# Performance work log

Measured on AMD Instinct MI355X. Metric: run time of the kernel, lower is better.

The kernel has to match this reference:

```python
import jax, jax.numpy as jnp
import numpy as np

B, T, D, H, L, FF, SPLIT = 2, 4096, 256, 4 * 0 + 8, 4, 1024, 2048
HD = D // H
EPS = 1e-5


def _layernorm(x, s, b):
    mu = jnp.mean(x, axis=-1, keepdims=True)
    var = jnp.mean(jnp.square(x - mu), axis=-1, keepdims=True)
    return (x - mu) * jax.lax.rsqrt(var + EPS) * s + b


def setup_inputs() -> dict:
    key = jax.random.key(0)
    ks = jax.random.split(key, 10)
    sc = 0.02
    inp = {
        "rows": jax.random.normal(ks[0], (B, T, D), jnp.float32),
        "train_target_embeddings": jax.random.normal(ks[1], (B, SPLIT, D), jnp.float32),
        "Wq": sc * jax.random.normal(ks[2], (L, D, D), jnp.float32),
        "bq": jnp.zeros((L, D), jnp.float32),
        "Wk": sc * jax.random.normal(ks[3], (L, D, D), jnp.float32),
        "bk": jnp.zeros((L, D), jnp.float32),
        "Wv": sc * jax.random.normal(ks[4], (L, D, D), jnp.float32),
        "bv": jnp.zeros((L, D), jnp.float32),
        "Wo": sc * jax.random.normal(ks[5], (L, D, D), jnp.float32),
        "bo": jnp.zeros((L, D), jnp.float32),
        "W1": sc * jax.random.normal(ks[6], (L, D, FF), jnp.float32),
        "b1": jnp.zeros((L, FF), jnp.float32),
        "W2": sc * jax.random.normal(ks[7], (L, FF, D), jnp.float32),
        "b2": jnp.zeros((L, D), jnp.float32),
        "ln1_s": jnp.ones((L, D), jnp.float32),
        "ln1_b": jnp.zeros((L, D), jnp.float32),
        "ln2_s": jnp.ones((L, D), jnp.float32),
        "ln2_b": jnp.zeros((L, D), jnp.float32),
        "split": SPLIT,
    }
    return inp


def reference(rows, train_target_embeddings, Wq, bq, Wk, bk, Wv, bv, Wo, bo,
              W1, b1, W2, b2, ln1_s, ln1_b, ln2_s, ln2_b, split):
    # residual add of train target embeddings onto the train rows
    x = rows.at[:, :split, :].add(train_target_embeddings)
    t = x.shape[1]
    # allowed mask: every query can see all train columns; test queries also see themselves
    key_is_train = jnp.arange(t) < split                      # [T]
    allowed = key_is_train[None, :] | jnp.eye(t, dtype=bool)  # [T,T]
    neg = jnp.asarray(-1e9, x.dtype)
    scale = 1.0 / np.sqrt(HD)
    n_layers = Wq.shape[0]
    for l in range(n_layers):
        # multi-head attention with structured mask
        q = (x @ Wq[l] + bq[l]).reshape(x.shape[0], t, H, HD)
        k = (x @ Wk[l] + bk[l]).reshape(x.shape[0], t, H, HD)
        v = (x @ Wv[l] + bv[l]).reshape(x.shape[0], t, H, HD)
        logits = jnp.einsum('bqhd,bkhd->bhqk', q, k) * scale
        logits = jnp.where(allowed[None, None], logits, neg)
        attn = jax.nn.softmax(logits, axis=-1)
        o = jnp.einsum('bhqk,bkhd->bqhd', attn, v).reshape(x.shape[0], t, D)
        x = _layernorm(x + (o @ Wo[l] + bo[l]), ln1_s[l], ln1_b[l])
        # feed-forward
        h = jax.nn.gelu(x @ W1[l] + b1[l])
        x = _layernorm(x + (h @ W2[l] + b2[l]), ln2_s[l], ln2_b[l])
    return x
```

## Files before the change

### kernel.cpp

```cpp
#include <hip/hip_runtime.h>
#include <cstdint>
#include <cstddef>

#define TSEQ 4096
#define BATCH 2
#define DIM 256
#define NHEAD 8
#define HDIM 32
#define NLAYER 4
#define FFDIM 1024
#define SPLITN 2048
#define MROWS (BATCH * TSEQ)

#define QSCALE 0.2550784545f

typedef __attribute__((ext_vector_type(4))) float f32x4;
typedef __attribute__((ext_vector_type(8))) short bf16x8;

__device__ __forceinline__ short f2bf(float f) {
  union { float f; uint32_t u; } v; v.f = f;
  uint32_t r = v.u + 0x7fffu + ((v.u >> 16) & 1u);
  return (short)(r >> 16);
}

__device__ __forceinline__ float fast_exp2(float x) {
#if __has_builtin(__builtin_amdgcn_exp2f)
  return __builtin_amdgcn_exp2f(x);
#else
  float r;
  asm volatile("v_exp_f32 %0, %1\n\ts_nop 1" : "=v"(r) : "v"(x));
  return r;
#endif
}

__device__ __forceinline__ uint32_t pack2bf(float a, float b) {
  union { float f; uint32_t u; } ua, ub; ua.f = a; ub.f = b;
  return ((ua.u + 0x8000u) >> 16) | ((ub.u + 0x8000u) & 0xffff0000u);
}

__device__ __forceinline__ float gelu_f(float x) {
  float u = 0.7978845608f * x * (1.0f + 0.044715f * x * x);
  u = fminf(fmaxf(u, -20.f), 20.f);
  float e = fast_exp2(2.885390082f * u);
  float t = (e - 1.0f) / (e + 1.0f);
  return 0.5f * x * (1.0f + t);
}

#define AS1 __attribute__((address_space(1)))
#define AS3 __attribute__((address_space(3)))
__device__ __forceinline__ void gload16(const void* g, void* l) {
  __builtin_amdgcn_global_load_lds((AS1 void*)g, (AS3 void*)l, 16, 0, 0);
}

__global__ __launch_bounds__(256) void prep_w(
    const float* __restrict__ Wq, const float* __restrict__ Wk,
    const float* __restrict__ Wv, const float* __restrict__ Wo,
    const float* __restrict__ W1, const float* __restrict__ W2,
    short* __restrict__ qkvT, short* __restrict__ woT,
    short* __restrict__ w1T, short* __restrict__ w2T)
{
  const int NQKV = NLAYER * 768 * DIM;
  const int NO   = NLAYER * DIM * DIM;
  const int NF   = NLAYER * FFDIM * DIM;
  const int total = NQKV + NO + 2 * NF;
  for (int idx = blockIdx.x * 256 + threadIdx.x; idx < total; idx += gridDim.x * 256) {
    if (idx < NQKV) {
      const int l = idx / (768 * DIM);
      const int rem = idx - l * 768 * DIM;
      const int n = rem >> 8, k = rem & 255;
      const float* src = (n < 256) ? Wq : ((n < 512) ? Wk : Wv);
      qkvT[idx] = f2bf(src[((size_t)l * DIM + k) * DIM + (n & 255)]);
    } else if (idx < NQKV + NO) {
      const int j = idx - NQKV;
      const int l = j >> 16;
      const int rem = j & 65535;
      const int n = rem >> 8, k = rem & 255;
      woT[j] = f2bf(Wo[((size_t)l * DIM + k) * DIM + n]);
    } else if (idx < NQKV + NO + NF) {
      const int j = idx - NQKV - NO;
      const int l = j >> 18;
      const int rem = j & 262143;
      const int n = rem >> 8, k = rem & 255;
      w1T[j] = f2bf(W1[((size_t)l * DIM + k) * FFDIM + n]);
    } else {
      const int j = idx - NQKV - NO - NF;
      const int l = j >> 18;
      const int rem = j & 262143;
      const int n = rem >> 10, k = rem & 1023;
      w2T[j] = f2bf(W2[((size_t)l * FFDIM + k) * DIM + n]);
    }
  }
}

__global__ __launch_bounds__(256) void prep_x(
    const float* __restrict__ rows, const float* __restrict__ tte,
    float* __restrict__ xf, short* __restrict__ xb)
{
  const size_t idx = (size_t)blockIdx.x * 256 + threadIdx.x;
  float4 v = ((const float4*)rows)[idx];
  const size_t e = idx * 4;
  const int m = (int)(e >> 8);
  const int d = (int)(e & 255);
  const int t = m & (TSEQ - 1);
  const int bb = m >> 12;
  if (t < SPLITN) {
    const float4 a = ((const float4*)tte)[((size_t)bb * SPLITN + t) * (DIM / 4) + (d >> 2)];
    v.x += a.x; v.y += a.y; v.z += a.z; v.w += a.w;
  }
  ((float4*)xf)[idx] = v;
  short4 pk; pk.x = f2bf(v.x); pk.y = f2bf(v.y); pk.z = f2bf(v.z); pk.w = f2bf(v.w);
  ((short4*)xb)[idx] = pk;
}

#define GBM 128
#define GBN 64
#define GBK 64

template<int EPI>
__global__ __launch_bounds__(256, 4) void gemm_bt(
    const short* __restrict__ A, const short* __restrict__ BT,
    const float* __restrict__ bias0, const float* __restrict__ bias1,
    const float* __restrict__ bias2, void* __restrict__ Cout,
    int M, int N, int K)
{
  __shared__ short As[GBM * GBK];
  __shared__ short Bs[GBN * GBK];
  const int tid = threadIdx.x;
  const int lane = tid & 63;
  const int wave = tid >> 6;
  const int wm = wave & 1, wn = wave >> 1;
  const int col = lane & 15, quad = lane >> 4;

  const short* Ab = A + (size_t)blockIdx.x * GBM * K;
  const short* Bb = BT + (size_t)blockIdx.y * GBN * K;

  const f32x4 fz = {0.f, 0.f, 0.f, 0.f};
  f32x4 acc[4][2];
#pragma unroll
  for (int i = 0; i < 4; ++i)
#pragma unroll
    for (int j = 0; j < 2; ++j) acc[i][j] = fz;

  for (int k0 = 0; k0 < K; k0 += GBK) {
#pragma unroll
    for (int p = 0; p < 4; ++p) {
      int i = p * 256 + tid;
      gload16(Ab + (size_t)(i >> 3) * K + k0 + (i & 7) * 8, &As[i * 8]);
    }
#pragma unroll
    for (int p = 0; p < 2; ++p) {
      int i = p * 256 + tid;
      gload16(Bb + (size_t)(i >> 3) * K + k0 + (i & 7) * 8, &Bs[i * 8]);
    }
    __syncthreads();
#pragma unroll
    for (int ks = 0; ks < GBK; ks += 32) {
      bf16x8 af[4], bfr[2];
#pragma unroll
      for (int tm = 0; tm < 4; ++tm)
        af[tm] = *(const bf16x8*)&As[(wm * 64 + tm * 16 + col) * GBK + ks + quad * 8];
#pragma unroll
      for (int tn = 0; tn < 2; ++tn)
        bfr[tn] = *(const bf16x8*)&Bs[(wn * 32 + tn * 16 + col) * GBK + ks + quad * 8];
#pragma unroll
      for (int tm = 0; tm < 4; ++tm)
#pragma unroll
        for (int tn = 0; tn < 2; ++tn)
          acc[tm][tn] = __builtin_amdgcn_mfma_f32_16x16x32_bf16(af[tm], bfr[tn], acc[tm][tn], 0, 0, 0);
    }
    __syncthreads();
  }

#pragma unroll
  for (int tm = 0; tm < 4; ++tm) {
    const int mbase = blockIdx.x * GBM + wm * 64 + tm * 16 + quad * 4;
#pragma unroll
    for (int tn = 0; tn < 2; ++tn) {
      const int n = blockIdx.y * GBN + wn * 32 + tn * 16 + col;
      float bv;
      if (EPI == 1) bv = (n < 256) ? bias0[n] : ((n < 512) ? bias1[n - 256] : bias2[n - 512]);
      else          bv = bias0[n];
#pragma unroll
      for (int r = 0; r < 4; ++r) {
        float v = acc[tm][tn][r] + bv;
        size_t off = (size_t)(mbase + r) * N + n;
        if (EPI == 1) {
          if (n < 256) v *= QSCALE;
          ((short*)Cout)[off] = f2bf(v);
        } else if (EPI == 2) {
          ((float*)Cout)[off] = v;
        } else {
          ((short*)Cout)[off] = f2bf(gelu_f(v));
        }
      }
    }
  }
}

__global__ __launch_bounds__(256) void transpose_v(
    const short* __restrict__ qkv, short* __restrict__ vt)
{
  __shared__ short tile[32][33];
  const int t0 = blockIdx.x * 32;
  const int c0 = blockIdx.y * 32;
  const int b = blockIdx.z;
  const int tx = threadIdx.x & 31, ty = threadIdx.x >> 5;
#pragma unroll
  for (int i = 0; i < 4; ++i) {
    const int t = t0 + ty + i * 8;
    tile[ty + i * 8][tx] = qkv[(size_t)(b * TSEQ + t) * 768 + 512 + c0 + tx];
  }
  __syncthreads();
#pragma unroll
  for (int i = 0; i < 4; ++i) {
    const int c = c0 + ty + i * 8;
    vt[(size_t)(b * DIM + c) * TSEQ + t0 + tx] = tile[tx][ty + i * 8];
  }
}

#define AKT 64

__global__ __launch_bounds__(256, 4) void attn_kernel(
    const short* __restrict__ qkv, const short* __restrict__ vt,
    short* __restrict__ outp)
{
  __shared__ short Kbuf[2][AKT * HDIM];
  __shared__ short Vbuf[2][HDIM * AKT];
  __shared__ short Pall[4][32][72];

  const int tid = threadIdx.x;
  const int lane = tid & 63;
  const int wave = tid >> 6;
  const int col = lane & 15, quad = lane >> 4;
  const int bh = blockIdx.y;
  const int b = bh >> 3, h = bh & 7;
  const int q0 = blockIdx.x * 128 + wave * 32;

  short (*P)[72] = Pall[wave];

  const short* qbase = qkv + (size_t)b * TSEQ * 768 + h * HDIM;
  const short* kbase = qbase + 256;
  const short* vtb = vt + (size_t)bh * HDIM * TSEQ;

  const short* ksrc = kbase + (size_t)(tid >> 2) * 768 + (tid & 3) * 8;
  const short* vsrc = vtb + (size_t)(tid >> 3) * TSEQ + (((tid & 7) ^ ((tid >> 3) & 7)) * 8);

  const bf16x8 qf0 = *(const bf16x8*)(qbase + (size_t)(q0 + col) * 768 + quad * 8);
  const bf16x8 qf1 = *(const bf16x8*)(qbase + (size_t)(q0 + 16 + col) * 768 + quad * 8);

  bf16x8 ones;
#pragma unroll
  for (int i = 0; i < 8; ++i) ones[i] = (short)0x3F80;

  const f32x4 fz = {0.f, 0.f, 0.f, 0.f};
  f32x4 o[2][2] = {{fz, fz}, {fz, fz}};
  f32x4 lacc0 = fz, lacc1 = fz;

  gload16(ksrc, &Kbuf[0][tid * 8]);
  gload16(vsrc, &Vbuf[0][tid * 8]);

  int cur = 0;
  for (int t = 0; t < SPLITN / AKT; ++t) {
    __syncthreads();
    if (t + 1 < SPLITN / AKT) {
      const int kn = (t + 1) * AKT;
      gload16(ksrc + (size_t)kn * 768, &Kbuf[1 - cur][tid * 8]);
      gload16(vsrc + kn, &Vbuf[1 - cur][tid * 8]);
    }
    const short* kb = Kbuf[cur];
    const short* vb = Vbuf[cur];

#pragma unroll
    for (int st = 0; st < 4; ++st) {
      const bf16x8 kf = *(const bf16x8*)&kb[(st * 16 + col) * HDIM + quad * 8];
      const f32x4 s0 = __builtin_amdgcn_mfma_f32_16x16x32_bf16(kf, qf0, fz, 0, 0, 0);
      const f32x4 s1 = __builtin_amdgcn_mfma_f32_16x16x32_bf16(kf, qf1, fz, 0, 0, 0);
      uint2 w0, w1;
      w0.x = pack2bf(fast_exp2(s0[0]), fast_exp2(s0[1]));
      w0.y = pack2bf(fast_exp2(s0[2]), fast_exp2(s0[3]));
      w1.x = pack2bf(fast_exp2(s1[0]), fast_exp2(s1[1]));
      w1.y = pack2bf(fast_exp2(s1[2]), fast_exp2(s1[3]));
      *(uint2*)&P[col][st * 16 + quad * 4] = w0;
      *(uint2*)&P[16 + col][st * 16 + quad * 4] = w1;
    }
    asm volatile("s_waitcnt lgkmcnt(0)" ::: "memory");

#pragma unroll
    for (int kh = 0; kh < 2; ++kh) {
      const bf16x8 pf0 = *(const bf16x8*)&P[col][kh * 32 + quad * 8];
      const bf16x8 pf1 = *(const bf16x8*)&P[16 + col][kh * 32 + quad * 8];
#pragma unroll
      for (int hh = 0; hh < 2; ++hh) {
        const int hd = hh * 16 + col;
        const bf16x8 vf = *(const bf16x8*)&vb[hd * AKT + (((kh * 4 + quad) ^ (hd & 7)) * 8)];
        o[0][hh] = __builtin_amdgcn_mfma_f32_16x16x32_bf16(pf0, vf, o[0][hh], 0, 0, 0);
        o[1][hh] = __builtin_amdgcn_mfma_f32_16x16x32_bf16(pf1, vf, o[1][hh], 0, 0, 0);
      }
      lacc0 = __builtin_amdgcn_mfma_f32_16x16x32_bf16(pf0, ones, lacc0, 0, 0, 0);
      lacc1 = __builtin_amdgcn_mfma_f32_16x16x32_bf16(pf1, ones, lacc1, 0, 0, 0);
    }
    cur ^= 1;
  }

  if (blockIdx.x >= SPLITN / 128) {
#pragma unroll
    for (int qsub = 0; qsub < 2; ++qsub) {
      const int qd = q0 + qsub * 16;
      const bf16x8 qf = qsub ? qf1 : qf0;
      const bf16x8 kf = *(const bf16x8*)(kbase + (size_t)(qd + col) * 768 + quad * 8);
      const f32x4 sd = __builtin_amdgcn_mfma_f32_16x16x32_bf16(kf, qf, fz, 0, 0, 0);
      float pd[4];
#pragma unroll
      for (int r = 0; r < 4; ++r)
        pd[r] = (quad * 4 + r) == col ? fast_exp2(sd[r]) : 0.f;
      uint2 w0, wz; wz.x = 0; wz.y = 0;
      w0.x = pack2bf(pd[0], pd[1]); w0.y = pack2bf(pd[2], pd[3]);
      *(uint2*)&P[qsub * 16 + col][quad * 4] = w0;
      *(uint2*)&P[qsub * 16 + col][16 + quad * 4] = wz;
    }
    asm volatile("s_waitcnt lgkmcnt(0)" ::: "memory");
#pragma unroll
    for (int qsub = 0; qsub < 2; ++qsub) {
      const int qd = q0 + qsub * 16;
      const bf16x8 pf = *(const bf16x8*)&P[qsub * 16 + col][quad * 8];
#pragma unroll
      for (int hh = 0; hh < 2; ++hh) {
        const bf16x8 vf = *(const bf16x8*)(vtb + (size_t)(hh * 16 + col) * TSEQ + qd + quad * 8);
        o[qsub][hh] = __builtin_amdgcn_mfma_f32_16x16x32_bf16(pf, vf, o[qsub][hh], 0, 0, 0);
      }
      if (qsub == 0) lacc0 = __builtin_amdgcn_mfma_f32_16x16x32_bf16(pf, ones, lacc0, 0, 0, 0);
      else           lacc1 = __builtin_amdgcn_mfma_f32_16x16x32_bf16(pf, ones, lacc1, 0, 0, 0);
    }
  }

#pragma unroll
  for (int qsub = 0; qsub < 2; ++qsub) {
    const f32x4 la = qsub ? lacc1 : lacc0;
    const int rowb = b * TSEQ + q0 + qsub * 16 + quad * 4;
#pragma unroll
    for (int r = 0; r < 4; ++r) {
      const float linv = 1.0f / la[r];
#pragma unroll
      for (int hh = 0; hh < 2; ++hh)
        outp[(size_t)(rowb + r) * DIM + h * HDIM + hh * 16 + col] = f2bf(o[qsub][hh][r] * linv);
    }
  }
}

__global__ __launch_bounds__(256) void ln_kernel(
    const float* __restrict__ xin, const float* __restrict__ proj,
    const float* __restrict__ gs, const float* __restrict__ gb,
    float* __restrict__ xoutf, short* __restrict__ xoutb)
{
  const int wave = threadIdx.x >> 6, lane = threadIdx.x & 63;
  const int row = blockIdx.x * 4 + wave;
  const float4 xv = *(const float4*)(xin + (size_t)row * DIM + lane * 4);
  const float4 pv = *(const float4*)(proj + (size_t)row * DIM + lane * 4);
  const float y0 = xv.x + pv.x, y1 = xv.y + pv.y, y2 = xv.z + pv.z, y3 = xv.w + pv.w;
  float s = y0 + y1 + y2 + y3;
  float q = y0 * y0 + y1 * y1 + y2 * y2 + y3 * y3;
#pragma unroll
  for (int o = 1; o < 64; o <<= 1) { s += __shfl_xor(s, o); q += __shfl_xor(q, o); }
  const float mu = s * (1.0f / DIM);
  const float var = q * (1.0f / DIM) - mu * mu;
  const float rstd = rsqrtf(var + 1e-5f);
  const float4 sv = *(const float4*)(gs + lane * 4);
  const float4 bv = *(const float4*)(gb + lane * 4);
  const float o0 = (y0 - mu) * rstd * sv.x + bv.x;
  const float o1 = (y1 - mu) * rstd * sv.y + bv.y;
  const float o2 = (y2 - mu) * rstd * sv.z + bv.z;
  const float o3 = (y3 - mu) * rstd * sv.w + bv.w;
  *(float4*)(xoutf + (size_t)row * DIM + lane * 4) = make_float4(o0, o1, o2, o3);
  short4 pk; pk.x = f2bf(o0); pk.y = f2bf(o1); pk.z = f2bf(o2); pk.w = f2bf(o3);
  *(short4*)(xoutb + (size_t)row * DIM + lane * 4) = pk;
}

extern "C" void kernel_launch(void* const* d_in, const int* in_sizes, int n_in,
                              void* d_out, int out_size, void* d_ws, size_t ws_size,
                              hipStream_t stream)
{
  const float* rows = (const float*)d_in[0];
  const float* tte  = (const float*)d_in[1];
  const float* Wq = (const float*)d_in[2];  const float* bq = (const float*)d_in[3];
  const float* Wk = (const float*)d_in[4];  const float* bk = (const float*)d_in[5];
  const float* Wv = (const float*)d_in[6];  const float* bv = (const float*)d_in[7];
  const float* Wo = (const float*)d_in[8];  const float* bo = (const float*)d_in[9];
  const float* W1 = (const float*)d_in[10]; const float* b1 = (const float*)d_in[11];
  const float* W2 = (const float*)d_in[12]; const float* b2 = (const float*)d_in[13];
  const float* ln1s = (const float*)d_in[14]; const float* ln1b = (const float*)d_in[15];
  const float* ln2s = (const float*)d_in[16]; const float* ln2b = (const float*)d_in[17];

  char* p = (char*)d_ws;
  float* xf   = (float*)p;  p += (size_t)MROWS * DIM * 4;
  short* xb   = (short*)p;  p += (size_t)MROWS * DIM * 2;
  short* qkv  = (short*)p;  p += (size_t)MROWS * 768 * 2;
  short* vtb  = (short*)p;  p += (size_t)BATCH * DIM * TSEQ * 2;
  short* ob   = (short*)p;  p += (size_t)MROWS * DIM * 2;
  float* tmpf = (float*)p;  p += (size_t)MROWS * DIM * 4;
  short* hb   = (short*)p;  p += (size_t)MROWS * FFDIM * 2;
  short* qkvT = (short*)p;  p += (size_t)NLAYER * 768 * DIM * 2;
  short* woT  = (short*)p;  p += (size_t)NLAYER * DIM * DIM * 2;
  short* w1T  = (short*)p;  p += (size_t)NLAYER * FFDIM * DIM * 2;
  short* w2T  = (short*)p;  p += (size_t)NLAYER * DIM * FFDIM * 2;

  prep_w<<<2048, 256, 0, stream>>>(Wq, Wk, Wv, Wo, W1, W2, qkvT, woT, w1T, w2T);
  prep_x<<<MROWS * DIM / 4 / 256, 256, 0, stream>>>(rows, tte, xf, xb);

  for (int l = 0; l < NLAYER; ++l) {
    gemm_bt<1><<<dim3(MROWS / GBM, 768 / GBN), 256, 0, stream>>>(
        xb, qkvT + (size_t)l * 768 * DIM, bq + l * DIM, bk + l * DIM, bv + l * DIM,
        qkv, MROWS, 768, DIM);
    transpose_v<<<dim3(TSEQ / 32, DIM / 32, BATCH), 256, 0, stream>>>(qkv, vtb);
    attn_kernel<<<dim3(TSEQ / 128, BATCH * NHEAD), 256, 0, stream>>>(qkv, vtb, ob);
    gemm_bt<2><<<dim3(MROWS / GBM, DIM / GBN), 256, 0, stream>>>(
        ob, woT + (size_t)l * DIM * DIM, bo + l * DIM, nullptr, nullptr,
        tmpf, MROWS, DIM, DIM);
    ln_kernel<<<MROWS / 4, 256, 0, stream>>>(xf, tmpf, ln1s + l * DIM, ln1b + l * DIM, xf, xb);
    gemm_bt<3><<<dim3(MROWS / GBM, FFDIM / GBN), 256, 0, stream>>>(
        xb, w1T + (size_t)l * FFDIM * DIM, b1 + l * FFDIM, nullptr, nullptr,
        hb, MROWS, FFDIM, DIM);
    gemm_bt<2><<<dim3(MROWS / GBM, DIM / GBN), 256, 0, stream>>>(
        hb, w2T + (size_t)l * DIM * FFDIM, b2 + l * DIM, nullptr, nullptr,
        tmpf, MROWS, DIM, FFDIM);
    float* xo = (l == NLAYER - 1) ? (float*)d_out : xf;
    ln_kernel<<<MROWS / 4, 256, 0, stream>>>(xf, tmpf, ln2s + l * DIM, ln2b + l * DIM, xo, xb);
  }
}
```

Before: 541.3 us.

## Fuse output GEMMs with LayerNorm and split attention keys across two blocks

Adds a gemm_ln kernel that computes a full 256-column row tile, then adds bias and residual and applies LayerNorm in the epilogue. This replaces both the gemm_bt<2> plus ln_kernel pairs and removes the fp32 tmpf round trip. Attention is split over two halves of the train keys (blockIdx.z) to double the number of blocks, with unnormalized partial outputs and row sums written in fp32. A new attn_combine kernel merges the two halves and normalizes. The K shared-memory layout also changes. In exchange this adds extra fp32 partial-output traffic and an extra launch, and gemm_ln runs without double buffering.

```diff
diff --git a/kernel.cpp b/kernel.cpp
--- a/kernel.cpp
+++ b/kernel.cpp
@@ -187,14 +187,115 @@
         if (EPI == 1) {
           if (n < 256) v *= QSCALE;
           ((short*)Cout)[off] = f2bf(v);
-        } else if (EPI == 2) {
-          ((float*)Cout)[off] = v;
         } else {
           ((short*)Cout)[off] = f2bf(gelu_f(v));
         }
       }
     }
   }
+}
+
+__global__ __launch_bounds__(256, 3) void gemm_ln(
+    const short* __restrict__ A, const short* __restrict__ BT,
+    const float* __restrict__ bias, const float* __restrict__ xres,
+    const float* __restrict__ gs, const float* __restrict__ gb,
+    float* __restrict__ xoutf, short* __restrict__ xoutb, int K)
+{
+  __shared__ short As[32 * 64];
+  __shared__ short Bs[256 * 64];
+  __shared__ float ssum[4][32], ssq[4][32];
+  const int tid = threadIdx.x;
+  const int lane = tid & 63;
+  const int wave = tid >> 6;
+  const int col = lane & 15, quad = lane >> 4;
+  const int m0 = blockIdx.x * 32;
+  const short* Ab = A + (size_t)m0 * K;
+
+  const f32x4 fz = {0.f, 0.f, 0.f, 0.f};
+  f32x4 acc[2][4];
+#pragma unroll
+  for (int i = 0; i < 2; ++i)
+#pragma unroll
+    for (int j = 0; j < 4; ++j) acc[i][j] = fz;
+
+  for (int k0 = 0; k0 < K; k0 += 64) {
+    gload16(Ab + (size_t)(tid >> 3) * K + k0 + (tid & 7) * 8, &As[tid * 8]);
+#pragma unroll
+    for (int p = 0; p < 8; ++p) {
+      int i = p * 256 + tid;
+      gload16(BT + (size_t)(i >> 3) * K + k0 + (i & 7) * 8, &Bs[i * 8]);
+    }
+    __syncthreads();
+#pragma unroll
+    for (int ks = 0; ks < 64; ks += 32) {
+      bf16x8 af[2], bfr[4];
+#pragma unroll
+      for (int tm = 0; tm < 2; ++tm)
+        af[tm] = *(const bf16x8*)&As[(tm * 16 + col) * 64 + ks + quad * 8];
+#pragma unroll
+      for (int tn = 0; tn < 4; ++tn)
+        bfr[tn] = *(const bf16x8*)&Bs[(wave * 64 + tn * 16 + col) * 64 + ks + quad * 8];
+#pragma unroll
+      for (int tm = 0; tm < 2; ++tm)
+#pragma unroll
+        for (int tn = 0; tn < 4; ++tn)
+          acc[tm][tn] = __builtin_amdgcn_mfma_f32_16x16x32_bf16(af[tm], bfr[tn], acc[tm][tn], 0, 0, 0);
+    }
+    __syncthreads();
+  }
+
+  const float* resb = xres + (size_t)m0 * DIM;
+#pragma unroll
+  for (int tn = 0; tn < 4; ++tn) {
+    const int n = wave * 64 + tn * 16 + col;
+    const float bv = bias[n];
+#pragma unroll
+    for (int tm = 0; tm < 2; ++tm)
+#pragma unroll
+      for (int r = 0; r < 4; ++r) {
+        const int row = tm * 16 + quad * 4 + r;
+        acc[tm][tn][r] += bv + resb[(size_t)row * DIM + n];
+      }
+  }
+
+#pragma unroll
+  for (int tm = 0; tm < 2; ++tm)
+#pragma unroll
+    for (int r = 0; r < 4; ++r) {
+      float s = 0.f, q = 0.f;
+#pragma unroll
+      for (int tn = 0; tn < 4; ++tn) { const float v = acc[tm][tn][r]; s += v; q += v * v; }
+      s += __shfl_xor(s, 1); q += __shfl_xor(q, 1);
+      s += __shfl_xor(s, 2); q += __shfl_xor(q, 2);
+      s += __shfl_xor(s, 4); q += __shfl_xor(q, 4);
+      s += __shfl_xor(s, 8); q += __shfl_xor(q, 8);
+      if (col == 0) { const int row = tm * 16 + quad * 4 + r; ssum[wave][row] = s; ssq[wave][row] = q; }
+    }
+  __syncthreads();
+  if (tid < 32) {
+    const float S = ssum[0][tid] + ssum[1][tid] + ssum[2][tid] + ssum[3][tid];
+    const float Q = ssq[0][tid] + ssq[1][tid] + ssq[2][tid] + ssq[3][tid];
+    const float mu = S * (1.0f / DIM);
+    const float var = Q * (1.0f / DIM) - mu * mu;
+    ssum[0][tid] = mu;
+    ssq[0][tid] = rsqrtf(var + 1e-5f);
+  }
+  __syncthreads();
+
+#pragma unroll
+  for (int tm = 0; tm < 2; ++tm)
+#pragma unroll
+    for (int tn = 0; tn < 4; ++tn) {
+      const int n = wave * 64 + tn * 16 + col;
+      const float g = gs[n], bb = gb[n];
+#pragma unroll
+      for (int r = 0; r < 4; ++r) {
+        const int row = tm * 16 + quad * 4 + r;
+        const float out = (acc[tm][tn][r] - ssum[0][row]) * ssq[0][row] * g + bb;
+        xoutf[(size_t)(m0 + row) * DIM + n] = out;
+        xoutb[(size_t)(m0 + row) * DIM + n] = f2bf(out);
+      }
+    }
 }
 
 __global__ __launch_bounds__(256) void transpose_v(
@@ -219,10 +320,11 @@
 }
 
 #define AKT 64
+#define KSPL 1024
 
 __global__ __launch_bounds__(256, 4) void attn_kernel(
     const short* __restrict__ qkv, const short* __restrict__ vt,
-    short* __restrict__ outp)
+    float* __restrict__ Opart, float* __restrict__ lpart)
 {
   __shared__ short Kbuf[2][AKT * HDIM];
   __shared__ short Vbuf[2][HDIM * AKT];
@@ -234,6 +336,7 @@
   const int col = lane & 15, quad = lane >> 4;
   const int bh = blockIdx.y;
   const int b = bh >> 3, h = bh & 7;
+  const int hz = blockIdx.z;
   const int q0 = blockIdx.x * 128 + wave * 32;
 
   short (*P)[72] = Pall[wave];
@@ -242,8 +345,8 @@
   const short* kbase = qbase + 256;
   const short* vtb = vt + (size_t)bh * HDIM * TSEQ;
 
-  const short* ksrc = kbase + (size_t)(tid >> 2) * 768 + (tid & 3) * 8;
-  const short* vsrc = vtb + (size_t)(tid >> 3) * TSEQ + (((tid & 7) ^ ((tid >> 3) & 7)) * 8);
+  const short* ksrc = kbase + (size_t)(hz * KSPL + (tid & 63)) * 768 + (tid >> 6) * 8;
+  const short* vsrc = vtb + (size_t)(tid >> 3) * TSEQ + hz * KSPL + (((tid & 7) ^ ((tid >> 3) & 7)) * 8);
 
   const bf16x8 qf0 = *(const bf16x8*)(qbase + (size_t)(q0 + col) * 768 + quad * 8);
   const bf16x8 qf1 = *(const bf16x8*)(qbase + (size_t)(q0 + 16 + col) * 768 + quad * 8);
@@ -260,9 +363,9 @@
   gload16(vsrc, &Vbuf[0][tid * 8]);
 
   int cur = 0;
-  for (int t = 0; t < SPLITN / AKT; ++t) {
+  for (int t = 0; t < KSPL / AKT; ++t) {
     __syncthreads();
-    if (t + 1 < SPLITN / AKT) {
+    if (t + 1 < KSPL / AKT) {
       const int kn = (t + 1) * AKT;
       gload16(ksrc + (size_t)kn * 768, &Kbuf[1 - cur][tid * 8]);
       gload16(vsrc + kn, &Vbuf[1 - cur][tid * 8]);
@@ -272,7 +375,7 @@
 
 #pragma unroll
     for (int st = 0; st < 4; ++st) {
-      const bf16x8 kf = *(const bf16x8*)&kb[(st * 16 + col) * HDIM + quad * 8];
+      const bf16x8 kf = *(const bf16x8*)&kb[(quad * 64 + st * 16 + col) * 8];
       const f32x4 s0 = __builtin_amdgcn_mfma_f32_16x16x32_bf16(kf, qf0, fz, 0, 0, 0);
       const f32x4 s1 = __builtin_amdgcn_mfma_f32_16x16x32_bf16(kf, qf1, fz, 0, 0, 0);
       uint2 w0, w1;
@@ -302,7 +405,7 @@
     cur ^= 1;
   }
 
-  if (blockIdx.x >= SPLITN / 128) {
+  if (hz == 1 && blockIdx.x >= SPLITN / 128) {
 #pragma unroll
     for (int qsub = 0; qsub < 2; ++qsub) {
       const int qd = q0 + qsub * 16;
@@ -333,46 +436,41 @@
     }
   }
 
+  float* Ob = Opart + (size_t)hz * MROWS * DIM;
+  float* lb = lpart + (size_t)hz * 16 * TSEQ + (size_t)bh * TSEQ;
 #pragma unroll
   for (int qsub = 0; qsub < 2; ++qsub) {
     const f32x4 la = qsub ? lacc1 : lacc0;
-    const int rowb = b * TSEQ + q0 + qsub * 16 + quad * 4;
+    const int qq = q0 + qsub * 16 + quad * 4;
+    const int rowb = b * TSEQ + qq;
 #pragma unroll
     for (int r = 0; r < 4; ++r) {
-      const float linv = 1.0f / la[r];
+      if (col == 0) lb[qq + r] = la[r];
 #pragma unroll
       for (int hh = 0; hh < 2; ++hh)
-        outp[(size_t)(rowb + r) * DIM + h * HDIM + hh * 16 + col] = f2bf(o[qsub][hh][r] * linv);
-    }
-  }
-}
-
-__global__ __launch_bounds__(256) void ln_kernel(
-    const float* __restrict__ xin, const float* __restrict__ proj,
-    const float* __restrict__ gs, const float* __restrict__ gb,
-    float* __restrict__ xoutf, short* __restrict__ xoutb)
-{
-  const int wave = threadIdx.x >> 6, lane = threadIdx.x & 63;
-  const int row = blockIdx.x * 4 + wave;
-  const float4 xv = *(const float4*)(xin + (size_t)row * DIM + lane * 4);
-  const float4 pv = *(const float4*)(proj + (size_t)row * DIM + lane * 4);
-  const float y0 = xv.x + pv.x, y1 = xv.y + pv.y, y2 = xv.z + pv.z, y3 = xv.w + pv.w;
-  float s = y0 + y1 + y2 + y3;
-  float q = y0 * y0 + y1 * y1 + y2 * y2 + y3 * y3;
-#pragma unroll
-  for (int o = 1; o < 64; o <<= 1) { s += __shfl_xor(s, o); q += __shfl_xor(q, o); }
-  const float mu = s * (1.0f / DIM);
-  const float var = q * (1.0f / DIM) - mu * mu;
-  const float rstd = rsqrtf(var + 1e-5f);
-  const float4 sv = *(const float4*)(gs + lane * 4);
-  const float4 bv = *(const float4*)(gb + lane * 4);
-  const float o0 = (y0 - mu) * rstd * sv.x + bv.x;
-  const float o1 = (y1 - mu) * rstd * sv.y + bv.y;
-  const float o2 = (y2 - mu) * rstd * sv.z + bv.z;
-  const float o3 = (y3 - mu) * rstd * sv.w + bv.w;
-  *(float4*)(xoutf + (size_t)row * DIM + lane * 4) = make_float4(o0, o1, o2, o3);
-  short4 pk; pk.x = f2bf(o0); pk.y = f2bf(o1); pk.z = f2bf(o2); pk.w = f2bf(o3);
-  *(short4*)(xoutb + (size_t)row * DIM + lane * 4) = pk;
+        Ob[(size_t)(rowb + r) * DIM + h * HDIM + hh * 16 + col] = o[qsub][hh][r];
+    }
+  }
+}
+
+__global__ __launch_bounds__(256) void attn_combine(
+    const float* __restrict__ Opart, const float* __restrict__ lpart,
+    short* __restrict__ ob)
+{
+  const int idx4 = blockIdx.x * 256 + threadIdx.x;
+  const int row = idx4 >> 6, d4 = idx4 & 63;
+  const int h = d4 >> 3, b = row >> 12, t = row & (TSEQ - 1);
+  const int bh = b * 8 + h;
+  const float l = lpart[bh * TSEQ + t] + lpart[16 * TSEQ + bh * TSEQ + t];
+  const float4 o0 = ((const float4*)Opart)[idx4];
+  const float4 o1 = ((const float4*)Opart)[(size_t)MROWS * (DIM / 4) + idx4];
+  const float linv = 1.0f / l;
+  short4 pk;
+  pk.x = f2bf((o0.x + o1.x) * linv);
+  pk.y = f2bf((o0.y + o1.y) * linv);
+  pk.z = f2bf((o0.z + o1.z) * linv);
+  pk.w = f2bf((o0.w + o1.w) * linv);
+  ((short4*)ob)[idx4] = pk;
 }
 
 extern "C" void kernel_launch(void* const* d_in, const int* in_sizes, int n_in,
@@ -396,8 +494,9 @@
   short* qkv  = (short*)p;  p += (size_t)MROWS * 768 * 2;
   short* vtb  = (short*)p;  p += (size_t)BATCH * DIM * TSEQ * 2;
   short* ob   = (short*)p;  p += (size_t)MROWS * DIM * 2;
-  float* tmpf = (float*)p;  p += (size_t)MROWS * DIM * 4;
   short* hb   = (short*)p;  p += (size_t)MROWS * FFDIM * 2;
+  float* Opart = (float*)p; p += (size_t)2 * MROWS * DIM * 4;
+  float* lpart = (float*)p; p += (size_t)2 * 16 * TSEQ * 4;
   short* qkvT = (short*)p;  p += (size_t)NLAYER * 768 * DIM * 2;
   short* woT  = (short*)p;  p += (size_t)NLAYER * DIM * DIM * 2;
   short* w1T  = (short*)p;  p += (size_t)NLAYER * FFDIM * DIM * 2;
@@ -411,18 +510,17 @@
         xb, qkvT + (size_t)l * 768 * DIM, bq + l * DIM, bk + l * DIM, bv + l * DIM,
         qkv, MROWS, 768, DIM);
     transpose_v<<<dim3(TSEQ / 32, DIM / 32, BATCH), 256, 0, stream>>>(qkv, vtb);
-    attn_kernel<<<dim3(TSEQ / 128, BATCH * NHEAD), 256, 0, stream>>>(qkv, vtb, ob);
-    gemm_bt<2><<<dim3(MROWS / GBM, DIM / GBN), 256, 0, stream>>>(
-        ob, woT + (size_t)l * DIM * DIM, bo + l * DIM, nullptr, nullptr,
-        tmpf, MROWS, DIM, DIM);
-    ln_kernel<<<MROWS / 4, 256, 0, stream>>>(xf, tmpf, ln1s + l * DIM, ln1b + l * DIM, xf, xb);
+    attn_kernel<<<dim3(TSEQ / 128, BATCH * NHEAD, 2), 256, 0, stream>>>(qkv, vtb, Opart, lpart);
+    attn_combine<<<MROWS * DIM / 4 / 256, 256, 0, stream>>>(Opart, lpart, ob);
+    gemm_ln<<<MROWS / 32, 256, 0, stream>>>(
+        ob, woT + (size_t)l * DIM * DIM, bo + l * DIM, xf,
+        ln1s + l * DIM, ln1b + l * DIM, xf, xb, DIM);
     gemm_bt<3><<<dim3(MROWS / GBM, FFDIM / GBN), 256, 0, stream>>>(
         xb, w1T + (size_t)l * FFDIM * DIM, b1 + l * FFDIM, nullptr, nullptr,
         hb, MROWS, FFDIM, DIM);
-    gemm_bt<2><<<dim3(MROWS / GBM, DIM / GBN), 256, 0, stream>>>(
-        hb, w2T + (size_t)l * DIM * FFDIM, b2 + l * DIM, nullptr, nullptr,
-        tmpf, MROWS, DIM, FFDIM);
     float* xo = (l == NLAYER - 1) ? (float*)d_out : xf;
-    ln_kernel<<<MROWS / 4, 256, 0, stream>>>(xf, tmpf, ln2s + l * DIM, ln2b + l * DIM, xo, xb);
-  }
-}
+    gemm_ln<<<MROWS / 32, 256, 0, stream>>>(
+        hb, w2T + (size_t)l * DIM * FFDIM, b2 + l * DIM, xf,
+        ln2s + l * DIM, ln2b + l * DIM, xo, xb, FFDIM);
+  }
+}
```

New measurement: 530.2 us. 1.02x faster.
